# Kernel tuning notes

Hardware: AMD Instinct MI355X
Metric: run time of the kernel (lower is better)

The kernel has to match this reference:

```python
import jax, jax.numpy as jnp
import numpy as np

K = 8  # FLAGS.num_neighbors


def _knn_project(verts, pc_coords, pc_feat):
    """One projected_neighborhood stage.
    verts:     [N, 3]   mesh vertices (queries)
    pc_coords: [1, 3, M] point-cloud coordinates
    pc_feat:   [1, Df, M] point-cloud features
    Returns (coord_out [N,3], feat_out [N,Df]).
    """
    pts = pc_coords[0].T            # [M, 3]
    feats = pc_feat[0].T            # [M, Df]
    x2 = jnp.sum(verts * verts, axis=1, keepdims=True)      # [N, 1]
    y2 = jnp.sum(pts * pts, axis=1)[None, :]                 # [1, M]
    d2 = jnp.maximum(x2 + y2 - 2.0 * (verts @ pts.T), 0.0)   # [N, M]
    _, idx = jax.lax.top_k(-d2, K)                            # [N, K] nearest
    nbr = pts[idx]                                            # [N, K, 3]
    vec = nbr - verts[:, None, :]                             # vec_to_neighbors
    dist2 = jnp.sum(vec * vec, axis=2)                        # knn_dist^2 [N, K]
    w = 1.0 / (1.0 + dist2)                                   # inverse_square_dist weight
    coord_out = jnp.mean(vec * w[:, :, None], axis=1) + verts
    feat_out = jnp.mean(feats[idx] * w[:, :, None], axis=1)   # [N, Df]
    return coord_out, feat_out


def setup_inputs() -> dict:
    key = jax.random.key(0)
    ks = jax.random.split(key, 8)
    return {
        "inputs": jax.random.normal(ks[0], (4096, 3), dtype=jnp.float32),
        "pc0_coords": jax.random.normal(ks[1], (1, 3, 32768), dtype=jnp.float32),
        "pc1_coords": jax.random.normal(ks[2], (1, 3, 32768), dtype=jnp.float32),
        "pc1_feat": jax.random.normal(ks[3], (1, 64, 32768), dtype=jnp.float32),
        "pc2_coords": jax.random.normal(ks[4], (1, 3, 16384), dtype=jnp.float32),
        "pc2_feat": jax.random.normal(ks[5], (1, 128, 16384), dtype=jnp.float32),
        "pc3_coords": jax.random.normal(ks[6], (1, 3, 8192), dtype=jnp.float32),
        "pc3_feat": jax.random.normal(ks[7], (1, 256, 8192), dtype=jnp.float32),
    }


def reference(inputs, pc0_coords, pc1_coords, pc1_feat, pc2_coords, pc2_feat,
              pc3_coords, pc3_feat):
    # NOTE: the original computes stage_0 (coords only, features==coords) but
    # discards it; the output only uses stages 1..3 features. We skip it.
    _, f1 = _knn_project(inputs, pc1_coords, pc1_feat)
    _, f2 = _knn_project(inputs, pc2_coords, pc2_feat)
    _, f3 = _knn_project(inputs, pc3_coords, pc3_feat)
    return jnp.concatenate([inputs, f1, f2, f3], axis=1)  # [N, 3+64+128+256]
```

## Files before the change

kernel.cpp:

```cpp
#include <hip/hip_runtime.h>
#include <float.h>

#define NV 4096
#define OSTRIDE 451
#define NT 256
typedef unsigned long long u64;

struct Top8 {
    unsigned d0,d1,d2,d3,d4,d5,d6,d7;
    int      i0,i1,i2,i3,i4,i5,i6,i7;
};

__device__ __forceinline__ void top8_init(Top8& t) {
    t.d0=t.d1=t.d2=t.d3=t.d4=t.d5=t.d6=t.d7=0x7F7FFFFFu;
    t.i0=t.i1=t.i2=t.i3=t.i4=t.i5=t.i6=t.i7=0x7fffffff;
}

__device__ __forceinline__ void ins8s(Top8& t, unsigned cd, int cm) {
    bool b0 = cd < t.d0, b1 = cd < t.d1, b2 = cd < t.d2, b3 = cd < t.d3;
    bool b4 = cd < t.d4, b5 = cd < t.d5, b6 = cd < t.d6;
    t.d7 = b6 ? t.d6 : cd;                 t.i7 = b6 ? t.i6 : cm;
    t.d6 = b5 ? t.d5 : (b6 ? cd : t.d6);   t.i6 = b5 ? t.i5 : (b6 ? cm : t.i6);
    t.d5 = b4 ? t.d4 : (b5 ? cd : t.d5);   t.i5 = b4 ? t.i4 : (b5 ? cm : t.i5);
    t.d4 = b3 ? t.d3 : (b4 ? cd : t.d4);   t.i4 = b3 ? t.i3 : (b4 ? cm : t.i4);
    t.d3 = b2 ? t.d2 : (b3 ? cd : t.d3);   t.i3 = b2 ? t.i2 : (b3 ? cm : t.i3);
    t.d2 = b1 ? t.d1 : (b2 ? cd : t.d2);   t.i2 = b1 ? t.i1 : (b2 ? cm : t.i2);
    t.d1 = b0 ? t.d0 : (b1 ? cd : t.d1);   t.i1 = b0 ? t.i0 : (b1 ? cm : t.i1);
    t.d0 = b0 ? cd : t.d0;                 t.i0 = b0 ? cm : t.i0;
}

__device__ __forceinline__ void handle_s(u64 mask, float dj, int ibase,
                                         Top8& t, float& Tf) {
    while (mask) {
        int l = __builtin_ctzll(mask);
        mask &= mask - 1;
        int cm = ibase + l;
        if (cm < 8) continue;
        unsigned cd = (unsigned)__builtin_amdgcn_readlane(__float_as_uint(dj), l);
        if (cd < t.d7) {
            ins8s(t, cd, cm);
            Tf = __uint_as_float(t.d7);
            mask &= __ballot(dj < Tf);
        }
    }
}

template<int M>
__device__ __forceinline__ float wcalc(const float* __restrict__ pc, int m,
                                       float vx, float vy, float vz) {
    float qx = pc[m], qy = pc[M+m], qz = pc[2*M+m];
    float dx = __fsub_rn(qx, vx), dy = __fsub_rn(qy, vy), dz = __fsub_rn(qz, vz);
    float dist2 = __fadd_rn(__fadd_rn(__fmul_rn(dx,dx), __fmul_rn(dy,dy)),
                            __fmul_rn(dz,dz));
    return __fdiv_rn(1.0f, __fadd_rn(1.0f, dist2));
}

template<int M, int DF, int COFF, bool TR>
__device__ __forceinline__ void stage2v(
    const float* __restrict__ verts,
    const float* __restrict__ pc,
    const float* __restrict__ feat,
    const float* __restrict__ featT,
    float* __restrict__ out,
    int vbase, int lane)
{
    float vx[2], vy[2], vz[2];
#pragma unroll
    for (int u = 0; u < 2; ++u) {
        vx[u] = verts[(vbase+u)*3+0];
        vy[u] = verts[(vbase+u)*3+1];
        vz[u] = verts[(vbase+u)*3+2];
    }

    Top8 t0, t1;
    top8_init(t0); top8_init(t1);

#pragma unroll
    for (int q = 0; q < 8; ++q) {
        float sx = pc[q], sy = pc[M+q], sz = pc[2*M+q];
        {
            float dx=__fsub_rn(sx,vx[0]), dy=__fsub_rn(sy,vy[0]), dz=__fsub_rn(sz,vz[0]);
            float d = __fmaf_rn(dz,dz,__fmaf_rn(dy,dy,__fmul_rn(dx,dx)));
            unsigned cd = (unsigned)__builtin_amdgcn_readfirstlane(__float_as_uint(d));
            if (cd < t0.d7) ins8s(t0, cd, q);
        }
        {
            float dx=__fsub_rn(sx,vx[1]), dy=__fsub_rn(sy,vy[1]), dz=__fsub_rn(sz,vz[1]);
            float d = __fmaf_rn(dz,dz,__fmaf_rn(dy,dy,__fmul_rn(dx,dx)));
            unsigned cd = (unsigned)__builtin_amdgcn_readfirstlane(__float_as_uint(d));
            if (cd < t1.d7) ins8s(t1, cd, q);
        }
    }
    float T[2];
    T[0] = __uint_as_float(t0.d7);
    T[1] = __uint_as_float(t1.d7);

    const float* __restrict__ px = pc;
    const float* __restrict__ py = pc + M;
    const float* __restrict__ pz = pc + 2*M;

    float cx[4], cy[4], cz[4];
#pragma unroll
    for (int j = 0; j < 4; ++j) {
        cx[j] = px[64*j + lane]; cy[j] = py[64*j + lane]; cz[j] = pz[64*j + lane];
    }

    for (int ob = 0; ob < M; ob += 256) {
        int nb = (ob + 256 < M) ? ob + 256 : 0;
        float nx[4], ny[4], nz[4];
#pragma unroll
        for (int j = 0; j < 4; ++j) {
            nx[j] = px[nb + 64*j + lane];
            ny[j] = py[nb + 64*j + lane];
            nz[j] = pz[nb + 64*j + lane];
        }
        float d[2][4];
#pragma unroll
        for (int u = 0; u < 2; ++u)
#pragma unroll
            for (int j = 0; j < 4; ++j) {
                float dx = __fsub_rn(cx[j], vx[u]);
                float dy = __fsub_rn(cy[j], vy[u]);
                float dz = __fsub_rn(cz[j], vz[u]);
                d[u][j] = __fmaf_rn(dz,dz,__fmaf_rn(dy,dy,__fmul_rn(dx,dx)));
            }
        u64 msk[2][4]; u64 any = 0;
#pragma unroll
        for (int u = 0; u < 2; ++u)
#pragma unroll
            for (int j = 0; j < 4; ++j) {
                msk[u][j] = __ballot(d[u][j] < T[u]);
                any |= msk[u][j];
            }
        if (any) {
#pragma unroll
            for (int j = 0; j < 4; ++j)
                handle_s(msk[0][j], d[0][j], ob + 64*j, t0, T[0]);
#pragma unroll
            for (int j = 0; j < 4; ++j)
                handle_s(msk[1][j], d[1][j], ob + 64*j, t1, T[1]);
        }
#pragma unroll
        for (int j = 0; j < 4; ++j) { cx[j]=nx[j]; cy[j]=ny[j]; cz[j]=nz[j]; }
    }

    int m8[2][8];
    m8[0][0]=t0.i0; m8[0][1]=t0.i1; m8[0][2]=t0.i2; m8[0][3]=t0.i3;
    m8[0][4]=t0.i4; m8[0][5]=t0.i5; m8[0][6]=t0.i6; m8[0][7]=t0.i7;
    m8[1][0]=t1.i0; m8[1][1]=t1.i1; m8[1][2]=t1.i2; m8[1][3]=t1.i3;
    m8[1][4]=t1.i4; m8[1][5]=t1.i5; m8[1][6]=t1.i6; m8[1][7]=t1.i7;
#pragma unroll
    for (int u = 0; u < 2; ++u) {
        float w8[8];
#pragma unroll
        for (int k = 0; k < 8; ++k)
            w8[k] = wcalc<M>(pc, m8[u][k], vx[u], vy[u], vz[u]);
        const int n = vbase + u;
        for (int f = lane; f < DF; f += 64) {
            float e[8];
#pragma unroll
            for (int k = 0; k < 8; ++k) {
                float fv = TR ? featT[m8[u][k]*DF + f] : feat[f*M + m8[u][k]];
                e[k] = __fmul_rn(w8[k], fv);
            }
            float s = __fadd_rn(__fadd_rn(__fadd_rn(e[0],e[1]), __fadd_rn(e[2],e[3])),
                                __fadd_rn(__fadd_rn(e[4],e[5]), __fadd_rn(e[6],e[7])));
            out[n*OSTRIDE + COFF + f] = __fmul_rn(0.125f, s);
        }
    }
}

__global__ __launch_bounds__(256)
void tr_kernel(const float* __restrict__ f1, const float* __restrict__ f2,
               const float* __restrict__ f3, float* __restrict__ ws)
{
    __shared__ float s[64][65];
    int b = blockIdx.x;
    const float* src; float* dst; int M, DF, tm, tf;
    if (b < 512)       { src = f1; dst = ws;           M = 32768; DF = 64;  tm = b & 511;        tf = b >> 9; }
    else if (b < 1024) { src = f2; dst = ws + 2097152; M = 16384; DF = 128; tm = (b-512) & 255;  tf = (b-512) >> 8; }
    else               { src = f3; dst = ws + 4194304; M = 8192;  DF = 256; tm = (b-1024) & 127; tf = (b-1024) >> 7; }
    const int mb = tm*64, fb = tf*64;
    const int tid = threadIdx.x;
    const int a0 = tid & 63, a1 = tid >> 6;
#pragma unroll
    for (int i = 0; i < 16; ++i) {
        int ff = a1 + i*4;
        s[ff][a0] = src[(fb+ff)*M + mb + a0];
    }
    __syncthreads();
#pragma unroll
    for (int i = 0; i < 16; ++i) {
        int mm2 = a1 + i*4;
        dst[(mb+mm2)*DF + fb + a0] = s[a0][mm2];
    }
}

template<bool TR>
__global__ __launch_bounds__(NT, 6)
void gp_kernel(const float* __restrict__ verts,
               const float* __restrict__ pc1, const float* __restrict__ f1,
               const float* __restrict__ pc2, const float* __restrict__ f2,
               const float* __restrict__ pc3, const float* __restrict__ f3,
               const float* __restrict__ ws,
               float* __restrict__ out)
{
    int b = blockIdx.x;
    if (b < 1536) {
        const int lane = threadIdx.x & 63;
        const int wv   = threadIdx.x >> 6;
        if (b < 512) {
            stage2v<32768,  64,   3, TR>(verts, pc1, f1, ws,           out, (b*4 + wv)*2, lane);
        } else if (b < 1024) {
            stage2v<16384, 128,  67, TR>(verts, pc2, f2, ws + 2097152, out, ((b-512)*4 + wv)*2, lane);
        } else {
            stage2v< 8192, 256, 195, TR>(verts, pc3, f3, ws + 4194304, out, ((b-1024)*4 + wv)*2, lane);
        }
    } else {
        for (int i = threadIdx.x; i < NV*3; i += NT)
            out[(i/3)*OSTRIDE + (i % 3)] = verts[i];
    }
}

extern "C" void kernel_launch(void* const* d_in, const int* in_sizes, int n_in,
                              void* d_out, int out_size, void* d_ws, size_t ws_size,
                              hipStream_t stream) {
    const float* verts = (const float*)d_in[0];
    const float* pc1 = (const float*)d_in[2];
    const float* f1  = (const float*)d_in[3];
    const float* pc2 = (const float*)d_in[4];
    const float* f2  = (const float*)d_in[5];
    const float* pc3 = (const float*)d_in[6];
    const float* f3  = (const float*)d_in[7];
    float* out = (float*)d_out;
    float* ws  = (float*)d_ws;

    if (ws_size >= 6291456u * sizeof(float)) {
        tr_kernel<<<1536, 256, 0, stream>>>(f1, f2, f3, ws);
        gp_kernel<true><<<1537, NT, 0, stream>>>(verts, pc1, f1, pc2, f2, pc3, f3, ws, out);
    } else {
        gp_kernel<false><<<1537, NT, 0, stream>>>(verts, pc1, f1, pc2, f2, pc3, f3, ws, out);
    }
}
```

Baseline: 131.1 us.

## Rebalance KNN work: one vertex per wave for largest cloud, four for smallest

Adds a single-vertex-per-wave KNN path for the 32768-point stage, doubling its block count, and packs four vertices per wave for the 8192-point stage so each block carries roughly equal scan work. Occupancy hint raised from 6 to 7 blocks per SM. The aim is to balance the per-block load across the three stages and remove long-tail blocks from the big stage. In exchange, the largest stage reads the point cloud twice as often overall, and the occupancy hint may increase register pressure or cause spills.

```diff
diff --git a/kernel.cpp b/kernel.cpp
--- a/kernel.cpp
+++ b/kernel.cpp
@@ -58,10 +58,8 @@
 template<int M, int DF, int COFF, bool TR>
 __device__ __forceinline__ void stage2v(
     const float* __restrict__ verts,
-    const float* __restrict__ pc,
-    const float* __restrict__ feat,
-    const float* __restrict__ featT,
-    float* __restrict__ out,
+    const float* __restrict__ pc, const float* __restrict__ feat,
+    const float* __restrict__ featT, float* __restrict__ out,
     int vbase, int lane)
 {
     float vx[2], vy[2], vz[2];
@@ -74,7 +72,6 @@
 
     Top8 t0, t1;
     top8_init(t0); top8_init(t1);
-
 #pragma unroll
     for (int q = 0; q < 8; ++q) {
         float sx = pc[q], sy = pc[M+q], sz = pc[2*M+q];
@@ -167,6 +164,86 @@
                                 __fadd_rn(__fadd_rn(e[4],e[5]), __fadd_rn(e[6],e[7])));
             out[n*OSTRIDE + COFF + f] = __fmul_rn(0.125f, s);
         }
+    }
+}
+
+template<int M, int DF, int COFF, bool TR>
+__device__ __forceinline__ void stage1v(
+    const float* __restrict__ verts,
+    const float* __restrict__ pc, const float* __restrict__ feat,
+    const float* __restrict__ featT, float* __restrict__ out,
+    int n, int lane)
+{
+    const float vx = verts[n*3+0], vy = verts[n*3+1], vz = verts[n*3+2];
+
+    Top8 t0;
+    top8_init(t0);
+#pragma unroll
+    for (int q = 0; q < 8; ++q) {
+        float sx = pc[q], sy = pc[M+q], sz = pc[2*M+q];
+        float dx=__fsub_rn(sx,vx), dy=__fsub_rn(sy,vy), dz=__fsub_rn(sz,vz);
+        float d = __fmaf_rn(dz,dz,__fmaf_rn(dy,dy,__fmul_rn(dx,dx)));
+        unsigned cd = (unsigned)__builtin_amdgcn_readfirstlane(__float_as_uint(d));
+        if (cd < t0.d7) ins8s(t0, cd, q);
+    }
+    float T = __uint_as_float(t0.d7);
+
+    const float* __restrict__ px = pc;
+    const float* __restrict__ py = pc + M;
+    const float* __restrict__ pz = pc + 2*M;
+
+    float cx[4], cy[4], cz[4];
+#pragma unroll
+    for (int j = 0; j < 4; ++j) {
+        cx[j] = px[64*j + lane]; cy[j] = py[64*j + lane]; cz[j] = pz[64*j + lane];
+    }
+
+    for (int ob = 0; ob < M; ob += 256) {
+        int nb = (ob + 256 < M) ? ob + 256 : 0;
+        float nx[4], ny[4], nz[4];
+#pragma unroll
+        for (int j = 0; j < 4; ++j) {
+            nx[j] = px[nb + 64*j + lane];
+            ny[j] = py[nb + 64*j + lane];
+            nz[j] = pz[nb + 64*j + lane];
+        }
+        float d[4];
+#pragma unroll
+        for (int j = 0; j < 4; ++j) {
+            float dx = __fsub_rn(cx[j], vx);
+            float dy = __fsub_rn(cy[j], vy);
+            float dz = __fsub_rn(cz[j], vz);
+            d[j] = __fmaf_rn(dz,dz,__fmaf_rn(dy,dy,__fmul_rn(dx,dx)));
+        }
+        u64 msk[4]; u64 any = 0;
+#pragma unroll
+        for (int j = 0; j < 4; ++j) { msk[j] = __ballot(d[j] < T); any |= msk[j]; }
+        if (any) {
+#pragma unroll
+            for (int j = 0; j < 4; ++j)
+                handle_s(msk[j], d[j], ob + 64*j, t0, T);
+        }
+#pragma unroll
+        for (int j = 0; j < 4; ++j) { cx[j]=nx[j]; cy[j]=ny[j]; cz[j]=nz[j]; }
+    }
+
+    int m8[8];
+    m8[0]=t0.i0; m8[1]=t0.i1; m8[2]=t0.i2; m8[3]=t0.i3;
+    m8[4]=t0.i4; m8[5]=t0.i5; m8[6]=t0.i6; m8[7]=t0.i7;
+    float w8[8];
+#pragma unroll
+    for (int k = 0; k < 8; ++k)
+        w8[k] = wcalc<M>(pc, m8[k], vx, vy, vz);
+    for (int f = lane; f < DF; f += 64) {
+        float e[8];
+#pragma unroll
+        for (int k = 0; k < 8; ++k) {
+            float fv = TR ? featT[m8[k]*DF + f] : feat[f*M + m8[k]];
+            e[k] = __fmul_rn(w8[k], fv);
+        }
+        float s = __fadd_rn(__fadd_rn(__fadd_rn(e[0],e[1]), __fadd_rn(e[2],e[3])),
+                            __fadd_rn(__fadd_rn(e[4],e[5]), __fadd_rn(e[6],e[7])));
+        out[n*OSTRIDE + COFF + f] = __fmul_rn(0.125f, s);
     }
 }
 
@@ -197,7 +274,7 @@
 }
 
 template<bool TR>
-__global__ __launch_bounds__(NT, 6)
+__global__ __launch_bounds__(NT, 7)
 void gp_kernel(const float* __restrict__ verts,
                const float* __restrict__ pc1, const float* __restrict__ f1,
                const float* __restrict__ pc2, const float* __restrict__ f2,
@@ -206,15 +283,17 @@
                float* __restrict__ out)
 {
     int b = blockIdx.x;
-    if (b < 1536) {
+    if (b < 1792) {
         const int lane = threadIdx.x & 63;
         const int wv   = threadIdx.x >> 6;
-        if (b < 512) {
-            stage2v<32768,  64,   3, TR>(verts, pc1, f1, ws,           out, (b*4 + wv)*2, lane);
-        } else if (b < 1024) {
-            stage2v<16384, 128,  67, TR>(verts, pc2, f2, ws + 2097152, out, ((b-512)*4 + wv)*2, lane);
+        if (b < 1024) {
+            stage1v<32768,  64,   3, TR>(verts, pc1, f1, ws,           out, b*4 + wv, lane);
+        } else if (b < 1536) {
+            stage2v<16384, 128,  67, TR>(verts, pc2, f2, ws + 2097152, out, ((b-1024)*4 + wv)*2, lane);
         } else {
-            stage2v< 8192, 256, 195, TR>(verts, pc3, f3, ws + 4194304, out, ((b-1024)*4 + wv)*2, lane);
+            const int vb = (b-1536)*16 + wv*4;
+            stage2v< 8192, 256, 195, TR>(verts, pc3, f3, ws + 4194304, out, vb,     lane);
+            stage2v< 8192, 256, 195, TR>(verts, pc3, f3, ws + 4194304, out, vb + 2, lane);
         }
     } else {
         for (int i = threadIdx.x; i < NV*3; i += NT)
@@ -237,8 +316,8 @@
 
     if (ws_size >= 6291456u * sizeof(float)) {
         tr_kernel<<<1536, 256, 0, stream>>>(f1, f2, f3, ws);
-        gp_kernel<true><<<1537, NT, 0, stream>>>(verts, pc1, f1, pc2, f2, pc3, f3, ws, out);
+        gp_kernel<true><<<1793, NT, 0, stream>>>(verts, pc1, f1, pc2, f2, pc3, f3, ws, out);
     } else {
-        gp_kernel<false><<<1537, NT, 0, stream>>>(verts, pc1, f1, pc2, f2, pc3, f3, ws, out);
-    }
-}
+        gp_kernel<false><<<1793, NT, 0, stream>>>(verts, pc1, f1, pc2, f2, pc3, f3, ws, out);
+    }
+}
```

After: 159.9 us. +22.0%, slower.

## Prefilter kNN candidates with precomputed point norms and dot-product expansion

Applied to the files above, without the earlier changes.

Precomputes squared norms of each point-cloud point in the workspace and, in the scan loop, uses a cheaper ||y||^2 - 2x·y test (three FMAs per vertex) against a margin-adjusted threshold to gate candidates. Exact distances are recomputed only for lanes whose wave passes the filter, which should cut per-candidate ALU work in the hot loop. It adds an extra workspace array and load stream per tile, plus branch overhead. The small margin guards against rounding differences that could otherwise drop true neighbors.

```diff
diff --git a/kernel.cpp b/kernel.cpp
--- a/kernel.cpp
+++ b/kernel.cpp
@@ -4,6 +4,10 @@
 #define NV 4096
 #define OSTRIDE 451
 #define NT 256
+#define PN1OFF 6291456
+#define PN2OFF (6291456 + 32768)
+#define PN3OFF (6291456 + 49152)
+#define MARGIN 1e-3f
 typedef unsigned long long u64;
 
 struct Top8 {
@@ -55,12 +59,13 @@
     return __fdiv_rn(1.0f, __fadd_rn(1.0f, dist2));
 }
 
-template<int M, int DF, int COFF, bool TR>
+template<int M, int DF, int COFF, bool TR, bool PN>
 __device__ __forceinline__ void stage2v(
     const float* __restrict__ verts,
     const float* __restrict__ pc,
     const float* __restrict__ feat,
     const float* __restrict__ featT,
+    const float* __restrict__ pnArr,
     float* __restrict__ out,
     int vbase, int lane)
 {
@@ -74,7 +79,6 @@
 
     Top8 t0, t1;
     top8_init(t0); top8_init(t1);
-
 #pragma unroll
     for (int q = 0; q < 8; ++q) {
         float sx = pc[q], sy = pc[M+q], sz = pc[2*M+q];
@@ -95,53 +99,120 @@
     T[0] = __uint_as_float(t0.d7);
     T[1] = __uint_as_float(t1.d7);
 
+    float c0[2], c1[2], c2[2], v2m[2], Tg[2];
+    if constexpr (PN) {
+#pragma unroll
+        for (int u = 0; u < 2; ++u) {
+            c0[u] = __fmul_rn(-2.0f, vx[u]);
+            c1[u] = __fmul_rn(-2.0f, vy[u]);
+            c2[u] = __fmul_rn(-2.0f, vz[u]);
+            float v2 = __fadd_rn(__fadd_rn(__fmul_rn(vx[u],vx[u]), __fmul_rn(vy[u],vy[u])),
+                                 __fmul_rn(vz[u],vz[u]));
+            v2m[u] = __fsub_rn(v2, MARGIN);
+            Tg[u]  = __fsub_rn(T[u], v2m[u]);
+        }
+    }
+
     const float* __restrict__ px = pc;
     const float* __restrict__ py = pc + M;
     const float* __restrict__ pz = pc + 2*M;
 
-    float cx[4], cy[4], cz[4];
+    float cx[4], cy[4], cz[4], cn[4];
 #pragma unroll
     for (int j = 0; j < 4; ++j) {
         cx[j] = px[64*j + lane]; cy[j] = py[64*j + lane]; cz[j] = pz[64*j + lane];
+        if constexpr (PN) cn[j] = pnArr[64*j + lane];
     }
 
     for (int ob = 0; ob < M; ob += 256) {
         int nb = (ob + 256 < M) ? ob + 256 : 0;
-        float nx[4], ny[4], nz[4];
+        float nx[4], ny[4], nz[4], nn[4];
 #pragma unroll
         for (int j = 0; j < 4; ++j) {
             nx[j] = px[nb + 64*j + lane];
             ny[j] = py[nb + 64*j + lane];
             nz[j] = pz[nb + 64*j + lane];
-        }
-        float d[2][4];
-#pragma unroll
-        for (int u = 0; u < 2; ++u)
+            if constexpr (PN) nn[j] = pnArr[nb + 64*j + lane];
+        }
+        if constexpr (PN) {
+            float s0[4], s1[4];
 #pragma unroll
             for (int j = 0; j < 4; ++j) {
-                float dx = __fsub_rn(cx[j], vx[u]);
-                float dy = __fsub_rn(cy[j], vy[u]);
-                float dz = __fsub_rn(cz[j], vz[u]);
-                d[u][j] = __fmaf_rn(dz,dz,__fmaf_rn(dy,dy,__fmul_rn(dx,dx)));
-            }
-        u64 msk[2][4]; u64 any = 0;
-#pragma unroll
-        for (int u = 0; u < 2; ++u)
+                s0[j] = __fmaf_rn(cx[j], c0[0], __fmaf_rn(cy[j], c1[0],
+                        __fmaf_rn(cz[j], c2[0], cn[j])));
+                s1[j] = __fmaf_rn(cx[j], c0[1], __fmaf_rn(cy[j], c1[1],
+                        __fmaf_rn(cz[j], c2[1], cn[j])));
+            }
+            u64 g0[4], g1[4]; u64 any = 0;
 #pragma unroll
             for (int j = 0; j < 4; ++j) {
-                msk[u][j] = __ballot(d[u][j] < T[u]);
-                any |= msk[u][j];
-            }
-        if (any) {
-#pragma unroll
-            for (int j = 0; j < 4; ++j)
-                handle_s(msk[0][j], d[0][j], ob + 64*j, t0, T[0]);
-#pragma unroll
-            for (int j = 0; j < 4; ++j)
-                handle_s(msk[1][j], d[1][j], ob + 64*j, t1, T[1]);
-        }
-#pragma unroll
-        for (int j = 0; j < 4; ++j) { cx[j]=nx[j]; cy[j]=ny[j]; cz[j]=nz[j]; }
+                g0[j] = __ballot(s0[j] < Tg[0]);
+                g1[j] = __ballot(s1[j] < Tg[1]);
+                any |= g0[j] | g1[j];
+            }
+            if (any) {
+#pragma unroll
+                for (int j = 0; j < 4; ++j) {
+                    if (g0[j]) {
+                        float dx = __fsub_rn(cx[j], vx[0]);
+                        float dy = __fsub_rn(cy[j], vy[0]);
+                        float dz = __fsub_rn(cz[j], vz[0]);
+                        float d2x = __fmaf_rn(dz,dz,__fmaf_rn(dy,dy,__fmul_rn(dx,dx)));
+                        u64 em = __ballot(d2x < T[0]);
+                        if (em) {
+                            handle_s(em, d2x, ob + 64*j, t0, T[0]);
+                            Tg[0] = __fsub_rn(T[0], v2m[0]);
+                        }
+                    }
+                }
+#pragma unroll
+                for (int j = 0; j < 4; ++j) {
+                    if (g1[j]) {
+                        float dx = __fsub_rn(cx[j], vx[1]);
+                        float dy = __fsub_rn(cy[j], vy[1]);
+                        float dz = __fsub_rn(cz[j], vz[1]);
+                        float d2x = __fmaf_rn(dz,dz,__fmaf_rn(dy,dy,__fmul_rn(dx,dx)));
+                        u64 em = __ballot(d2x < T[1]);
+                        if (em) {
+                            handle_s(em, d2x, ob + 64*j, t1, T[1]);
+                            Tg[1] = __fsub_rn(T[1], v2m[1]);
+                        }
+                    }
+                }
+            }
+        } else {
+            float d[2][4];
+#pragma unroll
+            for (int u = 0; u < 2; ++u)
+#pragma unroll
+                for (int j = 0; j < 4; ++j) {
+                    float dx = __fsub_rn(cx[j], vx[u]);
+                    float dy = __fsub_rn(cy[j], vy[u]);
+                    float dz = __fsub_rn(cz[j], vz[u]);
+                    d[u][j] = __fmaf_rn(dz,dz,__fmaf_rn(dy,dy,__fmul_rn(dx,dx)));
+                }
+            u64 msk[2][4]; u64 any = 0;
+#pragma unroll
+            for (int u = 0; u < 2; ++u)
+#pragma unroll
+                for (int j = 0; j < 4; ++j) {
+                    msk[u][j] = __ballot(d[u][j] < T[u]);
+                    any |= msk[u][j];
+                }
+            if (any) {
+#pragma unroll
+                for (int j = 0; j < 4; ++j)
+                    handle_s(msk[0][j], d[0][j], ob + 64*j, t0, T[0]);
+#pragma unroll
+                for (int j = 0; j < 4; ++j)
+                    handle_s(msk[1][j], d[1][j], ob + 64*j, t1, T[1]);
+            }
+        }
+#pragma unroll
+        for (int j = 0; j < 4; ++j) {
+            cx[j]=nx[j]; cy[j]=ny[j]; cz[j]=nz[j];
+            if constexpr (PN) cn[j]=nn[j];
+        }
     }
 
     int m8[2][8];
@@ -172,10 +243,21 @@
 
 __global__ __launch_bounds__(256)
 void tr_kernel(const float* __restrict__ f1, const float* __restrict__ f2,
-               const float* __restrict__ f3, float* __restrict__ ws)
+               const float* __restrict__ f3,
+               const float* __restrict__ pc1, const float* __restrict__ pc2,
+               const float* __restrict__ pc3, float* __restrict__ ws)
 {
+    int b = blockIdx.x;
+    if (b >= 1536) {
+        int g = (b - 1536)*256 + threadIdx.x;
+        float x, y, z; float* dst;
+        if (g < 32768)      { x=pc1[g];       y=pc1[32768+g];  z=pc1[65536+g];  dst=&ws[PN1OFF+g]; }
+        else if (g < 49152) { int m=g-32768;  x=pc2[m]; y=pc2[16384+m]; z=pc2[32768+m]; dst=&ws[PN2OFF+m]; }
+        else                { int m=g-49152;  x=pc3[m]; y=pc3[8192+m];  z=pc3[16384+m]; dst=&ws[PN3OFF+m]; }
+        *dst = __fmaf_rn(z,z,__fmaf_rn(y,y,__fmul_rn(x,x)));
+        return;
+    }
     __shared__ float s[64][65];
-    int b = blockIdx.x;
     const float* src; float* dst; int M, DF, tm, tf;
     if (b < 512)       { src = f1; dst = ws;           M = 32768; DF = 64;  tm = b & 511;        tf = b >> 9; }
     else if (b < 1024) { src = f2; dst = ws + 2097152; M = 16384; DF = 128; tm = (b-512) & 255;  tf = (b-512) >> 8; }
@@ -196,7 +278,7 @@
     }
 }
 
-template<bool TR>
+template<bool TR, bool PN>
 __global__ __launch_bounds__(NT, 6)
 void gp_kernel(const float* __restrict__ verts,
                const float* __restrict__ pc1, const float* __restrict__ f1,
@@ -210,11 +292,11 @@
         const int lane = threadIdx.x & 63;
         const int wv   = threadIdx.x >> 6;
         if (b < 512) {
-            stage2v<32768,  64,   3, TR>(verts, pc1, f1, ws,           out, (b*4 + wv)*2, lane);
+            stage2v<32768,  64,   3, TR, PN>(verts, pc1, f1, ws,           ws+PN1OFF, out, (b*4 + wv)*2, lane);
         } else if (b < 1024) {
-            stage2v<16384, 128,  67, TR>(verts, pc2, f2, ws + 2097152, out, ((b-512)*4 + wv)*2, lane);
+            stage2v<16384, 128,  67, TR, PN>(verts, pc2, f2, ws + 2097152, ws+PN2OFF, out, ((b-512)*4 + wv)*2, lane);
         } else {
-            stage2v< 8192, 256, 195, TR>(verts, pc3, f3, ws + 4194304, out, ((b-1024)*4 + wv)*2, lane);
+            stage2v< 8192, 256, 195, TR, PN>(verts, pc3, f3, ws + 4194304, ws+PN3OFF, out, ((b-1024)*4 + wv)*2, lane);
         }
     } else {
         for (int i = threadIdx.x; i < NV*3; i += NT)
@@ -235,10 +317,15 @@
     float* out = (float*)d_out;
     float* ws  = (float*)d_ws;
 
-    if (ws_size >= 6291456u * sizeof(float)) {
-        tr_kernel<<<1536, 256, 0, stream>>>(f1, f2, f3, ws);
-        gp_kernel<true><<<1537, NT, 0, stream>>>(verts, pc1, f1, pc2, f2, pc3, f3, ws, out);
+    const size_t need_tr = 6291456ull * 4ull;
+    const size_t need_pn = (6291456ull + 57344ull) * 4ull;
+    if (ws_size >= need_pn) {
+        tr_kernel<<<1760, 256, 0, stream>>>(f1, f2, f3, pc1, pc2, pc3, ws);
+        gp_kernel<true, true><<<1537, NT, 0, stream>>>(verts, pc1, f1, pc2, f2, pc3, f3, ws, out);
+    } else if (ws_size >= need_tr) {
+        tr_kernel<<<1536, 256, 0, stream>>>(f1, f2, f3, pc1, pc2, pc3, ws);
+        gp_kernel<true, false><<<1537, NT, 0, stream>>>(verts, pc1, f1, pc2, f2, pc3, f3, ws, out);
     } else {
-        gp_kernel<false><<<1537, NT, 0, stream>>>(verts, pc1, f1, pc2, f2, pc3, f3, ws, out);
-    }
-}
+        gp_kernel<false, false><<<1537, NT, 0, stream>>>(verts, pc1, f1, pc2, f2, pc3, f3, ws, out);
+    }
+}
```

New measurement: 124.7 us. 4.9% less time.

## Prefilter KNN with packed float4 dot-product bound and rebalance stages

Applied to the files above, without the earlier changes.

Packs point coordinates and their squared norms into float4 in the workspace, so each candidate needs one vectorized load and a 3-FMA expanded-distance screen against a threshold with a safety margin. Exact distances are recomputed only for lanes that pass the screen. Stage 1 is split across two waves that each scan half the points and then merge their top-8 lists through shared memory, and stage 3 blocks each process two vertex pairs, evening out work across blocks. The fallback path for a small workspace is removed, so the kernel now assumes a larger workspace, and the margin-based screen relies on the margin being large enough for correctness.

```diff
diff --git a/kernel.cpp b/kernel.cpp
--- a/kernel.cpp
+++ b/kernel.cpp
@@ -4,6 +4,10 @@
 #define NV 4096
 #define OSTRIDE 451
 #define NT 256
+#define PK1OFF 6291456
+#define PK2OFF (6291456 + 131072)
+#define PK3OFF (6291456 + 196608)
+#define MARGIN 1e-3f
 typedef unsigned long long u64;
 
 struct Top8 {
@@ -29,13 +33,31 @@
     t.d0 = b0 ? cd : t.d0;                 t.i0 = b0 ? cm : t.i0;
 }
 
-__device__ __forceinline__ void handle_s(u64 mask, float dj, int ibase,
-                                         Top8& t, float& Tf) {
+__device__ __forceinline__ void ins8lex(Top8& t, unsigned cd, int cm) {
+    bool b0 = (cd < t.d0) || (cd == t.d0 && cm < t.i0);
+    bool b1 = (cd < t.d1) || (cd == t.d1 && cm < t.i1);
+    bool b2 = (cd < t.d2) || (cd == t.d2 && cm < t.i2);
+    bool b3 = (cd < t.d3) || (cd == t.d3 && cm < t.i3);
+    bool b4 = (cd < t.d4) || (cd == t.d4 && cm < t.i4);
+    bool b5 = (cd < t.d5) || (cd == t.d5 && cm < t.i5);
+    bool b6 = (cd < t.d6) || (cd == t.d6 && cm < t.i6);
+    t.d7 = b6 ? t.d6 : cd;                 t.i7 = b6 ? t.i6 : cm;
+    t.d6 = b5 ? t.d5 : (b6 ? cd : t.d6);   t.i6 = b5 ? t.i5 : (b6 ? cm : t.i6);
+    t.d5 = b4 ? t.d4 : (b5 ? cd : t.d5);   t.i5 = b4 ? t.i4 : (b5 ? cm : t.i5);
+    t.d4 = b3 ? t.d3 : (b4 ? cd : t.d4);   t.i4 = b3 ? t.i3 : (b4 ? cm : t.i4);
+    t.d3 = b2 ? t.d2 : (b3 ? cd : t.d3);   t.i3 = b2 ? t.i2 : (b3 ? cm : t.i3);
+    t.d2 = b1 ? t.d1 : (b2 ? cd : t.d2);   t.i2 = b1 ? t.i1 : (b2 ? cm : t.i2);
+    t.d1 = b0 ? t.d0 : (b1 ? cd : t.d1);   t.i1 = b0 ? t.i0 : (b1 ? cm : t.i1);
+    t.d0 = b0 ? cd : t.d0;                 t.i0 = b0 ? cm : t.i0;
+}
+
+__device__ __forceinline__ void handle_p(u64 mask, float dj, int ibase,
+                                         int seedlim, Top8& t, float& Tf) {
     while (mask) {
         int l = __builtin_ctzll(mask);
         mask &= mask - 1;
         int cm = ibase + l;
-        if (cm < 8) continue;
+        if (cm < seedlim) continue;
         unsigned cd = (unsigned)__builtin_amdgcn_readlane(__float_as_uint(dj), l);
         if (cd < t.d7) {
             ins8s(t, cd, cm);
@@ -55,14 +77,126 @@
     return __fdiv_rn(1.0f, __fadd_rn(1.0f, dist2));
 }
 
-template<int M, int DF, int COFF, bool TR>
-__device__ __forceinline__ void stage2v(
-    const float* __restrict__ verts,
-    const float* __restrict__ pc,
-    const float* __restrict__ feat,
-    const float* __restrict__ featT,
-    float* __restrict__ out,
-    int vbase, int lane)
+#define SCAN_PK_BODY(PKP, BASE, LEN)                                          \
+    {                                                                         \
+        float c0[2], c1[2], c2[2], v2m[2], Tg[2];                             \
+        _Pragma("unroll")                                                     \
+        for (int u = 0; u < 2; ++u) {                                         \
+            c0[u] = __fmul_rn(-2.0f, vx[u]);                                  \
+            c1[u] = __fmul_rn(-2.0f, vy[u]);                                  \
+            c2[u] = __fmul_rn(-2.0f, vz[u]);                                  \
+            float v2 = __fadd_rn(__fadd_rn(__fmul_rn(vx[u],vx[u]),            \
+                       __fmul_rn(vy[u],vy[u])), __fmul_rn(vz[u],vz[u]));      \
+            v2m[u] = __fsub_rn(v2, MARGIN);                                   \
+            Tg[u]  = __fsub_rn(T[u], v2m[u]);                                 \
+        }                                                                     \
+        float4 cp[4];                                                         \
+        _Pragma("unroll")                                                     \
+        for (int j = 0; j < 4; ++j) cp[j] = (PKP)[(BASE) + 64*j + lane];      \
+        for (int ob = 0; ob < (LEN); ob += 256) {                             \
+            int nb = (ob + 256 < (LEN)) ? ob + 256 : 0;                       \
+            float4 np[4];                                                     \
+            _Pragma("unroll")                                                 \
+            for (int j = 0; j < 4; ++j) np[j] = (PKP)[(BASE) + nb + 64*j + lane]; \
+            float s0[4], s1[4];                                               \
+            _Pragma("unroll")                                                 \
+            for (int j = 0; j < 4; ++j) {                                     \
+                s0[j] = __fmaf_rn(cp[j].x, c0[0], __fmaf_rn(cp[j].y, c1[0],   \
+                        __fmaf_rn(cp[j].z, c2[0], cp[j].w)));                 \
+                s1[j] = __fmaf_rn(cp[j].x, c0[1], __fmaf_rn(cp[j].y, c1[1],   \
+                        __fmaf_rn(cp[j].z, c2[1], cp[j].w)));                 \
+            }                                                                 \
+            u64 g0[4], g1[4]; u64 any = 0;                                    \
+            _Pragma("unroll")                                                 \
+            for (int j = 0; j < 4; ++j) {                                     \
+                g0[j] = __ballot(s0[j] < Tg[0]);                              \
+                g1[j] = __ballot(s1[j] < Tg[1]);                              \
+                any |= g0[j] | g1[j];                                         \
+            }                                                                 \
+            if (any) {                                                        \
+                _Pragma("unroll")                                             \
+                for (int j = 0; j < 4; ++j) {                                 \
+                    if (g0[j]) {                                              \
+                        float dx = __fsub_rn(cp[j].x, vx[0]);                 \
+                        float dy = __fsub_rn(cp[j].y, vy[0]);                 \
+                        float dz = __fsub_rn(cp[j].z, vz[0]);                 \
+                        float d2x = __fmaf_rn(dz,dz,__fmaf_rn(dy,dy,__fmul_rn(dx,dx))); \
+                        u64 em = __ballot(d2x < T[0]);                        \
+                        if (em) {                                             \
+                            handle_p(em, d2x, (BASE) + ob + 64*j, (BASE) + 8, t0, T[0]); \
+                            Tg[0] = __fsub_rn(T[0], v2m[0]);                  \
+                        }                                                     \
+                    }                                                         \
+                }                                                             \
+                _Pragma("unroll")                                             \
+                for (int j = 0; j < 4; ++j) {                                 \
+                    if (g1[j]) {                                              \
+                        float dx = __fsub_rn(cp[j].x, vx[1]);                 \
+                        float dy = __fsub_rn(cp[j].y, vy[1]);                 \
+                        float dz = __fsub_rn(cp[j].z, vz[1]);                 \
+                        float d2x = __fmaf_rn(dz,dz,__fmaf_rn(dy,dy,__fmul_rn(dx,dx))); \
+                        u64 em = __ballot(d2x < T[1]);                        \
+                        if (em) {                                             \
+                            handle_p(em, d2x, (BASE) + ob + 64*j, (BASE) + 8, t1, T[1]); \
+                            Tg[1] = __fsub_rn(T[1], v2m[1]);                  \
+                        }                                                     \
+                    }                                                         \
+                }                                                             \
+            }                                                                 \
+            _Pragma("unroll")                                                 \
+            for (int j = 0; j < 4; ++j) cp[j] = np[j];                        \
+        }                                                                     \
+    }
+
+#define SEED2(PCP, MM, BASE)                                                  \
+    _Pragma("unroll")                                                         \
+    for (int q = 0; q < 8; ++q) {                                             \
+        float sx = (PCP)[(BASE)+q], sy = (PCP)[(MM)+(BASE)+q], sz = (PCP)[2*(MM)+(BASE)+q]; \
+        {                                                                     \
+            float dx=__fsub_rn(sx,vx[0]), dy=__fsub_rn(sy,vy[0]), dz=__fsub_rn(sz,vz[0]); \
+            float d = __fmaf_rn(dz,dz,__fmaf_rn(dy,dy,__fmul_rn(dx,dx)));     \
+            unsigned cd = (unsigned)__builtin_amdgcn_readfirstlane(__float_as_uint(d)); \
+            if (cd < t0.d7) ins8s(t0, cd, (BASE)+q);                          \
+        }                                                                     \
+        {                                                                     \
+            float dx=__fsub_rn(sx,vx[1]), dy=__fsub_rn(sy,vy[1]), dz=__fsub_rn(sz,vz[1]); \
+            float d = __fmaf_rn(dz,dz,__fmaf_rn(dy,dy,__fmul_rn(dx,dx)));     \
+            unsigned cd = (unsigned)__builtin_amdgcn_readfirstlane(__float_as_uint(d)); \
+            if (cd < t1.d7) ins8s(t1, cd, (BASE)+q);                          \
+        }                                                                     \
+    }
+
+#define EMIT2(PCP, MM, DFV, COFFV)                                            \
+    {                                                                         \
+        int m8[2][8];                                                         \
+        m8[0][0]=t0.i0; m8[0][1]=t0.i1; m8[0][2]=t0.i2; m8[0][3]=t0.i3;       \
+        m8[0][4]=t0.i4; m8[0][5]=t0.i5; m8[0][6]=t0.i6; m8[0][7]=t0.i7;       \
+        m8[1][0]=t1.i0; m8[1][1]=t1.i1; m8[1][2]=t1.i2; m8[1][3]=t1.i3;       \
+        m8[1][4]=t1.i4; m8[1][5]=t1.i5; m8[1][6]=t1.i6; m8[1][7]=t1.i7;       \
+        _Pragma("unroll")                                                     \
+        for (int u = 0; u < 2; ++u) {                                         \
+            float w8[8];                                                      \
+            _Pragma("unroll")                                                 \
+            for (int k = 0; k < 8; ++k)                                       \
+                w8[k] = wcalc<(MM)>((PCP), m8[u][k], vx[u], vy[u], vz[u]);    \
+            const int n = vbase + u;                                          \
+            for (int f = lane; f < (DFV); f += 64) {                          \
+                float e[8];                                                   \
+                _Pragma("unroll")                                             \
+                for (int k = 0; k < 8; ++k)                                   \
+                    e[k] = __fmul_rn(w8[k], featT[m8[u][k]*(DFV) + f]);       \
+                float s = __fadd_rn(__fadd_rn(__fadd_rn(e[0],e[1]), __fadd_rn(e[2],e[3])), \
+                                    __fadd_rn(__fadd_rn(e[4],e[5]), __fadd_rn(e[6],e[7]))); \
+                out[n*OSTRIDE + (COFFV) + f] = __fmul_rn(0.125f, s);          \
+            }                                                                 \
+        }                                                                     \
+    }
+
+template<int M, int DF, int COFF>
+__device__ __forceinline__ void stage_full(
+    const float* __restrict__ verts, const float* __restrict__ pc,
+    const float* __restrict__ featT, const float4* __restrict__ pk,
+    float* __restrict__ out, int vbase, int lane)
 {
     float vx[2], vy[2], vz[2];
 #pragma unroll
@@ -71,111 +205,113 @@
         vy[u] = verts[(vbase+u)*3+1];
         vz[u] = verts[(vbase+u)*3+2];
     }
-
-    Top8 t0, t1;
-    top8_init(t0); top8_init(t1);
-
-#pragma unroll
-    for (int q = 0; q < 8; ++q) {
-        float sx = pc[q], sy = pc[M+q], sz = pc[2*M+q];
-        {
-            float dx=__fsub_rn(sx,vx[0]), dy=__fsub_rn(sy,vy[0]), dz=__fsub_rn(sz,vz[0]);
-            float d = __fmaf_rn(dz,dz,__fmaf_rn(dy,dy,__fmul_rn(dx,dx)));
-            unsigned cd = (unsigned)__builtin_amdgcn_readfirstlane(__float_as_uint(d));
-            if (cd < t0.d7) ins8s(t0, cd, q);
-        }
-        {
-            float dx=__fsub_rn(sx,vx[1]), dy=__fsub_rn(sy,vy[1]), dz=__fsub_rn(sz,vz[1]);
-            float d = __fmaf_rn(dz,dz,__fmaf_rn(dy,dy,__fmul_rn(dx,dx)));
-            unsigned cd = (unsigned)__builtin_amdgcn_readfirstlane(__float_as_uint(d));
-            if (cd < t1.d7) ins8s(t1, cd, q);
-        }
-    }
+    Top8 t0, t1; top8_init(t0); top8_init(t1);
+    SEED2(pc, M, 0)
     float T[2];
     T[0] = __uint_as_float(t0.d7);
     T[1] = __uint_as_float(t1.d7);
-
-    const float* __restrict__ px = pc;
-    const float* __restrict__ py = pc + M;
-    const float* __restrict__ pz = pc + 2*M;
-
-    float cx[4], cy[4], cz[4];
+    SCAN_PK_BODY(pk, 0, M)
+    EMIT2(pc, M, DF, COFF)
+}
+
+__global__ __launch_bounds__(NT, 7)
+void gp_eq(const float* __restrict__ verts,
+           const float* __restrict__ pc1, const float* __restrict__ pc2,
+           const float* __restrict__ pc3,
+           const float* __restrict__ ws, float* __restrict__ out)
+{
+    __shared__ unsigned smd[2][16];
+    __shared__ int      smi[2][16];
+    const int b = blockIdx.x;
+    if (b >= 1792) {
+        for (int i = threadIdx.x; i < NV*3; i += NT)
+            out[(i/3)*OSTRIDE + (i % 3)] = verts[i];
+        return;
+    }
+    const int lane = threadIdx.x & 63;
+    const int wv   = threadIdx.x >> 6;
+    const float* featT1 = ws;
+    const float* featT2 = ws + 2097152;
+    const float* featT3 = ws + 4194304;
+    const float4* pk1 = (const float4*)(ws + PK1OFF);
+    const float4* pk2 = (const float4*)(ws + PK2OFF);
+    const float4* pk3 = (const float4*)(ws + PK3OFF);
+
+    if (b < 1024) {
+        const int slot  = wv >> 1;
+        const int part  = wv & 1;
+        const int vbase = (b*2 + slot)*2;
+        const int base  = part * 16384;
+        const float* featT = featT1;
+        float vx[2], vy[2], vz[2];
 #pragma unroll
-    for (int j = 0; j < 4; ++j) {
-        cx[j] = px[64*j + lane]; cy[j] = py[64*j + lane]; cz[j] = pz[64*j + lane];
-    }
-
-    for (int ob = 0; ob < M; ob += 256) {
-        int nb = (ob + 256 < M) ? ob + 256 : 0;
-        float nx[4], ny[4], nz[4];
-#pragma unroll
-        for (int j = 0; j < 4; ++j) {
-            nx[j] = px[nb + 64*j + lane];
-            ny[j] = py[nb + 64*j + lane];
-            nz[j] = pz[nb + 64*j + lane];
+        for (int u = 0; u < 2; ++u) {
+            vx[u] = verts[(vbase+u)*3+0];
+            vy[u] = verts[(vbase+u)*3+1];
+            vz[u] = verts[(vbase+u)*3+2];
         }
-        float d[2][4];
-#pragma unroll
-        for (int u = 0; u < 2; ++u)
-#pragma unroll
-            for (int j = 0; j < 4; ++j) {
-                float dx = __fsub_rn(cx[j], vx[u]);
-                float dy = __fsub_rn(cy[j], vy[u]);
-                float dz = __fsub_rn(cz[j], vz[u]);
-                d[u][j] = __fmaf_rn(dz,dz,__fmaf_rn(dy,dy,__fmul_rn(dx,dx)));
+        Top8 t0, t1; top8_init(t0); top8_init(t1);
+        SEED2(pc1, 32768, base)
+        float T[2];
+        T[0] = __uint_as_float(t0.d7);
+        T[1] = __uint_as_float(t1.d7);
+        SCAN_PK_BODY(pk1, base, 16384)
+        if (part == 1 && lane == 0) {
+            smd[slot][0]=t0.d0; smd[slot][1]=t0.d1; smd[slot][2]=t0.d2; smd[slot][3]=t0.d3;
+            smd[slot][4]=t0.d4; smd[slot][5]=t0.d5; smd[slot][6]=t0.d6; smd[slot][7]=t0.d7;
+            smi[slot][0]=t0.i0; smi[slot][1]=t0.i1; smi[slot][2]=t0.i2; smi[slot][3]=t0.i3;
+            smi[slot][4]=t0.i4; smi[slot][5]=t0.i5; smi[slot][6]=t0.i6; smi[slot][7]=t0.i7;
+            smd[slot][8]=t1.d0; smd[slot][9]=t1.d1; smd[slot][10]=t1.d2; smd[slot][11]=t1.d3;
+            smd[slot][12]=t1.d4; smd[slot][13]=t1.d5; smd[slot][14]=t1.d6; smd[slot][15]=t1.d7;
+            smi[slot][8]=t1.i0; smi[slot][9]=t1.i1; smi[slot][10]=t1.i2; smi[slot][11]=t1.i3;
+            smi[slot][12]=t1.i4; smi[slot][13]=t1.i5; smi[slot][14]=t1.i6; smi[slot][15]=t1.i7;
+        }
+        __syncthreads();
+        if (part == 0) {
+#pragma unroll 1
+            for (int s = 0; s < 8; ++s) {
+                unsigned cd = __builtin_amdgcn_readfirstlane(smd[slot][s]);
+                int      cm = __builtin_amdgcn_readfirstlane(smi[slot][s]);
+                if (!((cd < t0.d7) || (cd == t0.d7 && cm < t0.i7))) break;
+                ins8lex(t0, cd, cm);
             }
-        u64 msk[2][4]; u64 any = 0;
-#pragma unroll
-        for (int u = 0; u < 2; ++u)
-#pragma unroll
-            for (int j = 0; j < 4; ++j) {
-                msk[u][j] = __ballot(d[u][j] < T[u]);
-                any |= msk[u][j];
+#pragma unroll 1
+            for (int s = 0; s < 8; ++s) {
+                unsigned cd = __builtin_amdgcn_readfirstlane(smd[slot][8+s]);
+                int      cm = __builtin_amdgcn_readfirstlane(smi[slot][8+s]);
+                if (!((cd < t1.d7) || (cd == t1.d7 && cm < t1.i7))) break;
+                ins8lex(t1, cd, cm);
             }
-        if (any) {
-#pragma unroll
-            for (int j = 0; j < 4; ++j)
-                handle_s(msk[0][j], d[0][j], ob + 64*j, t0, T[0]);
-#pragma unroll
-            for (int j = 0; j < 4; ++j)
-                handle_s(msk[1][j], d[1][j], ob + 64*j, t1, T[1]);
+            EMIT2(pc1, 32768, 64, 3)
         }
-#pragma unroll
-        for (int j = 0; j < 4; ++j) { cx[j]=nx[j]; cy[j]=ny[j]; cz[j]=nz[j]; }
-    }
-
-    int m8[2][8];
-    m8[0][0]=t0.i0; m8[0][1]=t0.i1; m8[0][2]=t0.i2; m8[0][3]=t0.i3;
-    m8[0][4]=t0.i4; m8[0][5]=t0.i5; m8[0][6]=t0.i6; m8[0][7]=t0.i7;
-    m8[1][0]=t1.i0; m8[1][1]=t1.i1; m8[1][2]=t1.i2; m8[1][3]=t1.i3;
-    m8[1][4]=t1.i4; m8[1][5]=t1.i5; m8[1][6]=t1.i6; m8[1][7]=t1.i7;
-#pragma unroll
-    for (int u = 0; u < 2; ++u) {
-        float w8[8];
-#pragma unroll
-        for (int k = 0; k < 8; ++k)
-            w8[k] = wcalc<M>(pc, m8[u][k], vx[u], vy[u], vz[u]);
-        const int n = vbase + u;
-        for (int f = lane; f < DF; f += 64) {
-            float e[8];
-#pragma unroll
-            for (int k = 0; k < 8; ++k) {
-                float fv = TR ? featT[m8[u][k]*DF + f] : feat[f*M + m8[u][k]];
-                e[k] = __fmul_rn(w8[k], fv);
-            }
-            float s = __fadd_rn(__fadd_rn(__fadd_rn(e[0],e[1]), __fadd_rn(e[2],e[3])),
-                                __fadd_rn(__fadd_rn(e[4],e[5]), __fadd_rn(e[6],e[7])));
-            out[n*OSTRIDE + COFF + f] = __fmul_rn(0.125f, s);
-        }
+    } else if (b < 1536) {
+        const int vbase = ((b-1024)*4 + wv)*2;
+        stage_full<16384, 128, 67>(verts, pc2, featT2, pk2, out, vbase, lane);
+    } else {
+        const int q = (b-1536)*4 + wv;
+        stage_full<8192, 256, 195>(verts, pc3, featT3, pk3, out, (q*2+0)*2, lane);
+        stage_full<8192, 256, 195>(verts, pc3, featT3, pk3, out, (q*2+1)*2, lane);
     }
 }
 
 __global__ __launch_bounds__(256)
 void tr_kernel(const float* __restrict__ f1, const float* __restrict__ f2,
-               const float* __restrict__ f3, float* __restrict__ ws)
+               const float* __restrict__ f3,
+               const float* __restrict__ pc1, const float* __restrict__ pc2,
+               const float* __restrict__ pc3, float* __restrict__ ws)
 {
+    int b = blockIdx.x;
+    if (b >= 1536) {
+        int g = (b - 1536)*256 + threadIdx.x;
+        float x, y, z; float4* dst;
+        if (g < 32768)      { x=pc1[g];      y=pc1[32768+g];  z=pc1[65536+g];  dst=(float4*)(ws+PK1OFF)+g; }
+        else if (g < 49152) { int m=g-32768; x=pc2[m]; y=pc2[16384+m]; z=pc2[32768+m]; dst=(float4*)(ws+PK2OFF)+m; }
+        else                { int m=g-49152; x=pc3[m]; y=pc3[8192+m];  z=pc3[16384+m]; dst=(float4*)(ws+PK3OFF)+m; }
+        float pn = __fmaf_rn(z,z,__fmaf_rn(y,y,__fmul_rn(x,x)));
+        *dst = make_float4(x, y, z, pn);
+        return;
+    }
     __shared__ float s[64][65];
-    int b = blockIdx.x;
     const float* src; float* dst; int M, DF, tm, tf;
     if (b < 512)       { src = f1; dst = ws;           M = 32768; DF = 64;  tm = b & 511;        tf = b >> 9; }
     else if (b < 1024) { src = f2; dst = ws + 2097152; M = 16384; DF = 128; tm = (b-512) & 255;  tf = (b-512) >> 8; }
@@ -193,32 +329,6 @@
     for (int i = 0; i < 16; ++i) {
         int mm2 = a1 + i*4;
         dst[(mb+mm2)*DF + fb + a0] = s[a0][mm2];
-    }
-}
-
-template<bool TR>
-__global__ __launch_bounds__(NT, 6)
-void gp_kernel(const float* __restrict__ verts,
-               const float* __restrict__ pc1, const float* __restrict__ f1,
-               const float* __restrict__ pc2, const float* __restrict__ f2,
-               const float* __restrict__ pc3, const float* __restrict__ f3,
-               const float* __restrict__ ws,
-               float* __restrict__ out)
-{
-    int b = blockIdx.x;
-    if (b < 1536) {
-        const int lane = threadIdx.x & 63;
-        const int wv   = threadIdx.x >> 6;
-        if (b < 512) {
-            stage2v<32768,  64,   3, TR>(verts, pc1, f1, ws,           out, (b*4 + wv)*2, lane);
-        } else if (b < 1024) {
-            stage2v<16384, 128,  67, TR>(verts, pc2, f2, ws + 2097152, out, ((b-512)*4 + wv)*2, lane);
-        } else {
-            stage2v< 8192, 256, 195, TR>(verts, pc3, f3, ws + 4194304, out, ((b-1024)*4 + wv)*2, lane);
-        }
-    } else {
-        for (int i = threadIdx.x; i < NV*3; i += NT)
-            out[(i/3)*OSTRIDE + (i % 3)] = verts[i];
     }
 }
 
@@ -235,10 +345,6 @@
     float* out = (float*)d_out;
     float* ws  = (float*)d_ws;
 
-    if (ws_size >= 6291456u * sizeof(float)) {
-        tr_kernel<<<1536, 256, 0, stream>>>(f1, f2, f3, ws);
-        gp_kernel<true><<<1537, NT, 0, stream>>>(verts, pc1, f1, pc2, f2, pc3, f3, ws, out);
-    } else {
-        gp_kernel<false><<<1537, NT, 0, stream>>>(verts, pc1, f1, pc2, f2, pc3, f3, ws, out);
-    }
-}
+    tr_kernel<<<1760, 256, 0, stream>>>(f1, f2, f3, pc1, pc2, pc3, ws);
+    gp_eq<<<1793, NT, 0, stream>>>(verts, pc1, pc2, pc3, ws, out);
+}
```

Measured after the change: 416.1 us. 217% more time.
